# Kernel tuning notes

Measured on AMD Instinct MI355X. Metric: run time of the kernel, lower is better.

The kernel has to match this reference:

```python
import jax, jax.numpy as jnp
import numpy as np

DIM = 128; PDIM = 32; WS = 16; HEADS = 4; NBLK = 2

def gelu(x):
    return jax.nn.gelu(x, approximate=False)  # torch default GELU (erf)

def conv2d(x, w, b=None, pad=0, groups=1):
    y = jax.lax.conv_general_dilated(x, w, (1, 1), [(pad, pad), (pad, pad)],
                                     feature_group_count=groups,
                                     dimension_numbers=('NCHW', 'OIHW', 'NCHW'))
    if b is not None:
        y = y + b[None, :, None, None]
    return y

def layernorm_cf(x, w, b, eps=1e-6):
    # channels_first LayerNorm over C per (b,h,w)
    m = x.mean(axis=1, keepdims=True)
    v = ((x - m) ** 2).mean(axis=1, keepdims=True)
    return (x - m) / jnp.sqrt(v + eps) * w[None, :, None, None] + b[None, :, None, None]

def conv_ffn(x, w1, b1, dw, dwb, w2, b2):
    y = gelu(conv2d(x, w1, b1, 0))
    y = gelu(conv2d(y, dw, dwb, 1, groups=y.shape[1])) + y
    return conv2d(y, w2, b2, 0)

def conv_attention(x, lk, pw1, pb1, pw2, pb2):
    # ConvolutionalAttention (training branch math, non-inplace)
    B, C, H, W = x.shape
    x1, x2 = x[:, :PDIM], x[:, PDIM:]
    # dwc_proj: global avg pool -> 1x1 -> GELU -> 1x1 (pure matmuls on pooled vec)
    v = x1.mean(axis=(2, 3))                              # [B, PDIM]
    h = gelu(v @ pw1[:, :, 0, 0].T + pb1)                 # [B, PDIM//2]
    dk = (h @ pw2[:, :, 0, 0].T + pb2).reshape(B * PDIM, 1, 3, 3)
    # per-sample dynamic depthwise conv via groups = B*PDIM
    dyn = conv2d(x1.reshape(1, B * PDIM, H, W), dk, None, 1,
                 groups=B * PDIM).reshape(B, PDIM, H, W)
    x1 = conv2d(x1, lk, None, lk.shape[-1] // 2) + dyn
    return jnp.concatenate([x1, x2], axis=1)

def window_attention(x, qkv_w, qkv_b, out_w, out_b, table):
    B, C, H, W = x.shape  # H,W divisible by WS -> pad_to_win is a no-op
    hd, wd = H // WS, W // WS
    c = C // HEADS
    qkv = conv2d(x, qkv_w, qkv_b, 0)                      # [B, 3C, H, W]
    qkv = qkv.reshape(B, 3, HEADS, c, hd, WS, wd, WS)
    qkv = qkv.transpose(1, 0, 4, 6, 2, 5, 7, 3).reshape(3, B * hd * wd, HEADS, WS * WS, c)
    q, k, v = qkv[0], qkv[1], qkv[2]
    S = WS * WS
    idx = jnp.arange(S); qh = idx // WS; qw = idx % WS
    rel = (qh[None, :] - qh[:, None] + WS - 1) * (2 * WS - 1) + (qw[None, :] - qw[:, None] + WS - 1)
    bias = table[:, rel]                                  # [HEADS, S, S]
    scores = jnp.einsum('nhqc,nhkc->nhqk', q, k) * (c ** -0.5) + bias[None]
    attn = jax.nn.softmax(scores, axis=-1)
    o = jnp.einsum('nhqk,nhkc->nhqc', attn, v)
    o = o.reshape(B, hd, wd, HEADS, WS, WS, c).transpose(0, 3, 6, 1, 4, 2, 5).reshape(B, C, H, W)
    return conv2d(o, out_w, out_b, 0)

def forward(x, plk_filter, ln_proj_w, ln_proj_b, proj_w1, proj_b1, proj_dw, proj_dwb,
            proj_w2, proj_b2, ln_attn_w, ln_attn_b, qkv_w, qkv_b, attn_out_w, attn_out_b,
            rpe_table, ffn_w1, ffn_b1, ffn_dw, ffn_dwb, ffn_w2, ffn_b2,
            pk_w1, pk_b1, pk_w2, pk_b2, pk_aggr_w, pk_aggr_b,
            ln_out_w, ln_out_b, co_w, co_b):
    skip = x
    x = layernorm_cf(x, ln_proj_w, ln_proj_b)
    x = conv_ffn(x, proj_w1, proj_b1, proj_dw, proj_dwb, proj_w2, proj_b2)
    x = x + window_attention(layernorm_cf(x, ln_attn_w, ln_attn_b),
                             qkv_w, qkv_b, attn_out_w, attn_out_b, rpe_table)
    for i in range(NBLK):
        y = conv_ffn(x, ffn_w1[i], ffn_b1[i], ffn_dw[i], ffn_dwb[i], ffn_w2[i], ffn_b2[i])
        y = conv_attention(y, plk_filter, pk_w1[i], pk_b1[i], pk_w2[i], pk_b2[i])
        y = conv2d(y, pk_aggr_w[i], pk_aggr_b[i], 0)
        x = x + y
    x = conv2d(layernorm_cf(x, ln_out_w, ln_out_b), co_w, co_b, 1)
    return x + skip

def setup_inputs() -> dict:
    key = jax.random.key(0)
    ks = iter(jax.random.split(key, 64))
    def rn(shape, s=0.02):
        return jax.random.normal(next(ks), shape, jnp.float32) * s
    d = DIM; e = 2 * d
    return dict(
        x=jax.random.normal(next(ks), (4, d, 192, 192), jnp.float32),
        plk_filter=rn((PDIM, PDIM, 13, 13), 0.05),
        ln_proj_w=jnp.ones((d,), jnp.float32), ln_proj_b=jnp.zeros((d,), jnp.float32),
        proj_w1=rn((e, d, 1, 1)), proj_b1=rn((e,)),
        proj_dw=rn((e, 1, 3, 3), 0.1), proj_dwb=rn((e,)),
        proj_w2=rn((d, e, 1, 1)), proj_b2=rn((d,)),
        ln_attn_w=jnp.ones((d,), jnp.float32), ln_attn_b=jnp.zeros((d,), jnp.float32),
        qkv_w=rn((3 * d, d, 1, 1)), qkv_b=rn((3 * d,)),
        attn_out_w=rn((d, d, 1, 1)), attn_out_b=rn((d,)),
        rpe_table=rn((HEADS, (2 * WS - 1) ** 2), 0.001),
        ffn_w1=rn((NBLK, e, d, 1, 1)), ffn_b1=rn((NBLK, e)),
        ffn_dw=rn((NBLK, e, 1, 3, 3), 0.1), ffn_dwb=rn((NBLK, e)),
        ffn_w2=rn((NBLK, d, e, 1, 1)), ffn_b2=rn((NBLK, d)),
        pk_w1=rn((NBLK, PDIM // 2, PDIM, 1, 1)), pk_b1=rn((NBLK, PDIM // 2)),
        pk_w2=rn((NBLK, PDIM * 9, PDIM // 2, 1, 1), 0.01), pk_b2=rn((NBLK, PDIM * 9), 0.01),
        pk_aggr_w=rn((NBLK, d, d, 1, 1)), pk_aggr_b=rn((NBLK, d)),
        ln_out_w=jnp.ones((d,), jnp.float32), ln_out_b=jnp.zeros((d,), jnp.float32),
        co_w=rn((d, d, 3, 3), 0.05), co_b=rn((d,)),
    )

def reference(x, plk_filter, ln_proj_w, ln_proj_b, proj_w1, proj_b1, proj_dw, proj_dwb,
              proj_w2, proj_b2, ln_attn_w, ln_attn_b, qkv_w, qkv_b, attn_out_w, attn_out_b,
              rpe_table, ffn_w1, ffn_b1, ffn_dw, ffn_dwb, ffn_w2, ffn_b2,
              pk_w1, pk_b1, pk_w2, pk_b2, pk_aggr_w, pk_aggr_b,
              ln_out_w, ln_out_b, co_w, co_b):
    return forward(x, plk_filter, ln_proj_w, ln_proj_b, proj_w1, proj_b1, proj_dw, proj_dwb,
                   proj_w2, proj_b2, ln_attn_w, ln_attn_b, qkv_w, qkv_b, attn_out_w, attn_out_b,
                   rpe_table, ffn_w1, ffn_b1, ffn_dw, ffn_dwb, ffn_w2, ffn_b2,
                   pk_w1, pk_b1, pk_w2, pk_b2, pk_aggr_w, pk_aggr_b,
                   ln_out_w, ln_out_b, co_w, co_b)
```

## Files before the change

### kernel.cpp

```cpp
#include <hip/hip_runtime.h>
#include <cmath>

#define HWD 192
#define PIX (HWD*HWD)
#define BB  4
#define CCH 128

using short8 = __attribute__((ext_vector_type(8))) short;
using f32x4  = __attribute__((ext_vector_type(4))) float;

__device__ __forceinline__ float gelu_f(float x) {
    return 0.5f * x * (1.0f + erff(x * 0.70710678118654752f));
}
__device__ __forceinline__ unsigned short f2bf(float f) {
    unsigned int u = __float_as_uint(f);
    u += 0x7fff + ((u >> 16) & 1);
    return (unsigned short)(u >> 16);
}
__device__ __forceinline__ float bf2f(unsigned short s) {
    return __uint_as_float((unsigned int)s << 16);
}
__device__ __forceinline__ unsigned short to_bf(float v) { return f2bf(v); }
__device__ __forceinline__ unsigned short to_bf(unsigned short v) { return v; }
__device__ __forceinline__ unsigned pack2bf(float a, float b) {
    return (unsigned)f2bf(a) | ((unsigned)f2bf(b) << 16);
}

__global__ __launch_bounds__(256) void ln_kernel(const float* __restrict__ in,
        const float* __restrict__ w, const float* __restrict__ b,
        unsigned short* __restrict__ out)
{
    int t = blockIdx.x * 256 + threadIdx.x;
    int bi = t / PIX;
    int p  = t - bi*PIX;
    const float* base = in + (size_t)bi * CCH * PIX + p;
    float v[CCH];
    float s = 0.f;
    #pragma unroll
    for (int c=0;c<CCH;++c) { v[c] = base[(size_t)c*PIX]; s += v[c]; }
    float m = s * (1.f/128.f);
    float q = 0.f;
    #pragma unroll
    for (int c=0;c<CCH;++c) { float d = v[c]-m; q += d*d; }
    float iv = rsqrtf(q*(1.f/128.f) + 1e-6f);
    unsigned short* ob = out + (size_t)bi * CCH * PIX + p;
    #pragma unroll
    for (int c=0;c<CCH;++c)
        ob[(size_t)c*PIX] = f2bf((v[c]-m)*iv*w[c] + b[c]);
}

__global__ __launch_bounds__(256) void ln_t_kernel(const float* __restrict__ in,
        const float* __restrict__ w, const float* __restrict__ b,
        unsigned short* __restrict__ outT)
{
    int t = blockIdx.x * 256 + threadIdx.x;
    int bi = t / PIX;
    int p  = t - bi*PIX;
    const float* base = in + (size_t)bi * CCH * PIX + p;
    float v[CCH];
    float s = 0.f;
    #pragma unroll
    for (int c=0;c<CCH;++c) { v[c] = base[(size_t)c*PIX]; s += v[c]; }
    float m = s * (1.f/128.f);
    float q = 0.f;
    #pragma unroll
    for (int c=0;c<CCH;++c) { float d = v[c]-m; q += d*d; }
    float iv = rsqrtf(q*(1.f/128.f) + 1e-6f);
    unsigned short* ob = outT + ((size_t)bi * PIX + p) * 128;
    #pragma unroll
    for (int qq=0; qq<16; ++qq) {
        unsigned short e[8];
        #pragma unroll
        for (int j=0;j<8;++j) {
            int c = qq*8 + j;
            e[j] = f2bf((v[c]-m)*iv*w[c] + b[c]);
        }
        *(uint4*)&ob[qq*8] = *(uint4*)e;
    }
}

__global__ __launch_bounds__(256) void t32_kernel(const unsigned short* __restrict__ in,
    unsigned short* __restrict__ outT)
{
    int t = blockIdx.x * 256 + threadIdx.x;
    int bi = t / PIX;
    int p  = t - bi*PIX;
    const unsigned short* base = in + (size_t)bi * CCH * PIX + p;
    unsigned short e[32];
    #pragma unroll
    for (int c=0;c<32;++c) e[c] = base[(size_t)c*PIX];
    unsigned short* ob = outT + ((size_t)bi * PIX + p) * 32;
    #pragma unroll
    for (int q=0;q<4;++q) *(uint4*)&ob[q*8] = *(uint4*)&e[q*8];
}

template<typename TIN, bool DOGELU, bool DORES, bool OBF>
__global__ __launch_bounds__(256) void conv1x1_mfma_kernel(
    const TIN* __restrict__ in,
    const unsigned short* __restrict__ wq,
    const float* __restrict__ bias,
    const float* __restrict__ res,
    void* __restrict__ outv,
    int Cin)
{
    constexpr int CIP = 72;
    __shared__ unsigned short XL[128*CIP];
    const int Cout = gridDim.y * 128;
    const int px0 = blockIdx.x * 128;
    const int co0 = blockIdx.y * 128;
    const size_t bi = blockIdx.z;
    in  += bi * (size_t)Cin * PIX;
    if (DORES) res += bi * (size_t)Cout * PIX;
    float* outf = (float*)outv + bi * (size_t)Cout * PIX;
    unsigned short* outb = (unsigned short*)outv + bi * (size_t)Cout * PIX;
    const int tid = threadIdx.x;
    const int lane = tid & 63, wid = tid >> 6;
    const int wco = (wid >> 1) * 64;
    const int wpx = (wid & 1) * 64;
    const int l15 = lane & 15, l4 = lane >> 4;

    f32x4 acc[4][4];
    #pragma unroll
    for (int i=0;i<4;++i)
        #pragma unroll
        for (int j=0;j<4;++j) acc[i][j] = (f32x4){0.f,0.f,0.f,0.f};

    for (int k0 = 0; k0 < Cin; k0 += 64) {
        __syncthreads();
        #pragma unroll
        for (int it = 0; it < 8; ++it) {
            int f = tid + it*256;
            int px = f & 127;
            int ci = (f >> 7) * 4;
            const TIN* gp = in + (size_t)(k0+ci)*PIX + px0 + px;
            unsigned short b0 = to_bf(gp[0]);
            unsigned short b1 = to_bf(gp[PIX]);
            unsigned short b2 = to_bf(gp[2*PIX]);
            unsigned short b3 = to_bf(gp[3*PIX]);
            uint2 pk;
            pk.x = (unsigned)b0 | ((unsigned)b1 << 16);
            pk.y = (unsigned)b2 | ((unsigned)b3 << 16);
            *(uint2*)&XL[px*CIP + ci] = pk;
        }
        __syncthreads();
        #pragma unroll
        for (int ks = 0; ks < 2; ++ks) {
            short8 a[4];
            #pragma unroll
            for (int mt=0; mt<4; ++mt) {
                int co = co0 + wco + mt*16 + l15;
                a[mt] = *(const short8*)(wq + (size_t)co*Cin + k0 + ks*32 + l4*8);
            }
            #pragma unroll
            for (int nt=0; nt<4; ++nt) {
                const short8 b = *(const short8*)&XL[(wpx + nt*16 + l15)*CIP + ks*32 + l4*8];
                #pragma unroll
                for (int mt=0; mt<4; ++mt)
                    acc[mt][nt] = __builtin_amdgcn_mfma_f32_16x16x32_bf16(a[mt], b, acc[mt][nt], 0, 0, 0);
            }
        }
    }
    #pragma unroll
    for (int mt=0; mt<4; ++mt) {
        #pragma unroll
        for (int r=0; r<4; ++r) {
            int co = co0 + wco + mt*16 + l4*4 + r;
            float bs = bias[co];
            #pragma unroll
            for (int nt=0; nt<4; ++nt) {
                int px = px0 + wpx + nt*16 + l15;
                float v = acc[mt][nt][r] + bs;
                if (DOGELU) v = gelu_f(v);
                size_t o = (size_t)co*PIX + px;
                if (DORES) v += res[o];
                if (OBF) outb[o] = f2bf(v);
                else     outf[o] = v;
            }
        }
    }
}

__global__ __launch_bounds__(256) void conv3x3_mfma_kernel(
    const unsigned short* __restrict__ inT,
    const unsigned short* __restrict__ wq,
    const float* __restrict__ bias, const float* __restrict__ skip,
    float* __restrict__ out)
{
    constexpr int CIP = 40;
    __shared__ unsigned short XL[4*66*CIP];
    const int x0 = blockIdx.x * 64;
    const int y0 = blockIdx.y * 2;
    const int bi = blockIdx.z;
    const int tid = threadIdx.x;
    const int lane = tid & 63, wid = tid >> 6;
    const int wco = (wid >> 1) * 64;
    const int wrow = wid & 1;
    const int l15 = lane & 15, l4 = lane >> 4;
    const unsigned short* inb = inT + (size_t)bi * PIX * 128;

    f32x4 acc[4][4];
    #pragma unroll
    for (int i=0;i<4;++i)
        #pragma unroll
        for (int j=0;j<4;++j) acc[i][j] = (f32x4){0.f,0.f,0.f,0.f};

    for (int ci0 = 0; ci0 < 128; ci0 += 32) {
        __syncthreads();
        #pragma unroll
        for (int it = 0; it < 5; ++it) {
            int idx = tid + it*256;
            if (idx < 1056) {
                int P = idx >> 2;
                int q = idx & 3;
                int row = P / 66;
                int x = P - row*66;
                int gy = y0 - 1 + row, gx = x0 - 1 + x;
                uint4 v = {0u,0u,0u,0u};
                if ((unsigned)gy < (unsigned)HWD && (unsigned)gx < (unsigned)HWD)
                    v = *(const uint4*)&inb[((size_t)gy*HWD + gx)*128 + ci0 + q*8];
                *(uint4*)&XL[(row*66 + x)*CIP + q*8] = v;
            }
        }
        __syncthreads();
        #pragma unroll
        for (int dy=0; dy<3; ++dy) {
            #pragma unroll
            for (int dx=0; dx<3; ++dx) {
                short8 a[4];
                #pragma unroll
                for (int mt=0; mt<4; ++mt) {
                    int co = wco + mt*16 + l15;
                    a[mt] = *(const short8*)(wq + ((size_t)co*9 + dy*3+dx)*128 + ci0 + l4*8);
                }
                const int rl = wrow + dy;
                #pragma unroll
                for (int nt=0; nt<4; ++nt) {
                    const int xl = nt*16 + l15 + dx;
                    const short8 b = *(const short8*)&XL[(rl*66 + xl)*CIP + l4*8];
                    #pragma unroll
                    for (int mt=0; mt<4; ++mt)
                        acc[mt][nt] = __builtin_amdgcn_mfma_f32_16x16x32_bf16(a[mt], b, acc[mt][nt], 0, 0, 0);
                }
            }
        }
    }
    const int gy = y0 + wrow;
    #pragma unroll
    for (int mt=0; mt<4; ++mt) {
        #pragma unroll
        for (int r=0; r<4; ++r) {
            int co = wco + mt*16 + l4*4 + r;
            float bs = bias[co];
            #pragma unroll
            for (int nt=0; nt<4; ++nt) {
                int gx = x0 + nt*16 + l15;
                size_t o = ((size_t)bi*CCH + co)*PIX + (size_t)gy*HWD + gx;
                out[o] = acc[mt][nt][r] + bs + skip[o];
            }
        }
    }
}

__global__ __launch_bounds__(256) void conv13_mfma_kernel(
    const unsigned short* __restrict__ YT,
    const unsigned short* __restrict__ wq,
    const float* __restrict__ dk,
    unsigned short* __restrict__ outC)
{
    __shared__ unsigned short XL[16*76*32];
    const int x0 = blockIdx.x * 64;
    const int y0 = blockIdx.y * 4;
    const int bi = blockIdx.z;
    const int tid = threadIdx.x;
    const int lane = tid & 63, wr = tid >> 6;
    const int l15 = lane & 15, l4 = lane >> 4;
    const unsigned short* inT = YT + (size_t)bi * PIX * 32;

    #pragma unroll 1
    for (int it = 0; it < 19; ++it) {
        int idx = tid + it*256;
        int P = idx >> 2;
        int q = idx & 3;
        int row = P / 76;
        int x   = P - row*76;
        int gy = y0 - 6 + row, gx = x0 - 6 + x;
        uint4 v = {0u,0u,0u,0u};
        if ((unsigned)gy < (unsigned)HWD && (unsigned)gx < (unsigned)HWD)
            v = *(const uint4*)&inT[((size_t)gy*HWD + gx)*32 + q*8];
        *(uint4*)&XL[P*32 + ((q*8) ^ ((P&3)<<3))] = v;
    }
    __syncthreads();

    f32x4 acc[2][4];
    #pragma unroll
    for (int i=0;i<2;++i)
        #pragma unroll
        for (int j=0;j<4;++j) acc[i][j] = (f32x4){0.f,0.f,0.f,0.f};

    #pragma unroll 1
    for (int dy=0; dy<13; ++dy) {
        const unsigned short* wrow = wq + (size_t)dy*13*1024;
        #pragma unroll
        for (int dx=0; dx<13; ++dx) {
            const short8 a0 = *(const short8*)(wrow + dx*1024 + l15*32 + l4*8);
            const short8 a1 = *(const short8*)(wrow + dx*1024 + (16+l15)*32 + l4*8);
            #pragma unroll
            for (int nt=0; nt<4; ++nt) {
                const int P = (wr + dy)*76 + nt*16 + l15 + dx;
                const short8 b = *(const short8*)&XL[P*32 + ((l4*8) ^ ((P&3)<<3))];
                acc[0][nt] = __builtin_amdgcn_mfma_f32_16x16x32_bf16(a0, b, acc[0][nt], 0, 0, 0);
                acc[1][nt] = __builtin_amdgcn_mfma_f32_16x16x32_bf16(a1, b, acc[1][nt], 0, 0, 0);
            }
        }
    }
    const int gy = y0 + wr;
    #pragma unroll
    for (int mt=0; mt<2; ++mt) {
        #pragma unroll
        for (int r=0; r<4; ++r) {
            const int co = mt*16 + l4*4 + r;
            const float* dkk = dk + (bi*32 + co)*9;
            float k0=dkk[0],k1=dkk[1],k2=dkk[2],k3=dkk[3],k4=dkk[4],
                  k5=dkk[5],k6=dkk[6],k7=dkk[7],k8=dkk[8];
            #pragma unroll
            for (int nt=0; nt<4; ++nt) {
                const int px = nt*16 + l15;
                float dsum = 0.f;
                #pragma unroll
                for (int e=0; e<9; ++e) {
                    int ey = e/3, ex = e - ey*3;
                    int P = (wr+5+ey)*76 + px+5+ex;
                    float pv = bf2f(XL[P*32 + (co ^ ((P&3)<<3))]);
                    float kk = (e==0?k0:e==1?k1:e==2?k2:e==3?k3:e==4?k4:e==5?k5:e==6?k6:e==7?k7:k8);
                    dsum += pv * kk;
                }
                float v = acc[mt][nt][r] + dsum;
                outC[((size_t)bi*32 + co)*PIX + (size_t)gy*HWD + x0 + px] = f2bf(v);
            }
        }
    }
}

__global__ __launch_bounds__(256) void dw3x3_bf_kernel(const unsigned short* __restrict__ in,
    const float* __restrict__ w, const float* __restrict__ b,
    unsigned short* __restrict__ out)
{
    int t = blockIdx.x*256 + threadIdx.x;
    int pc = t / (PIX/4);
    int p4 = (t - pc*(PIX/4)) * 4;
    int c = pc & 255;
    int y = p4 / HWD, x0 = p4 - y*HWD;
    const unsigned short* ib = in + (size_t)pc * PIX;
    float wk[9];
    #pragma unroll
    for (int e=0;e<9;++e) wk[e] = w[c*9+e];
    float bc = b[c];
    float a0=bc,a1=bc,a2=bc,a3=bc;
    #pragma unroll
    for (int ky=0;ky<3;++ky) {
        int yy = y + ky - 1;
        if ((unsigned)yy < (unsigned)HWD) {
            const unsigned short* row = ib + (size_t)yy*HWD;
            float v[6];
            #pragma unroll
            for (int d=0;d<6;++d) {
                int xx = x0 + d - 1;
                v[d] = ((unsigned)xx < (unsigned)HWD) ? bf2f(row[xx]) : 0.f;
            }
            a0 += v[0]*wk[ky*3+0] + v[1]*wk[ky*3+1] + v[2]*wk[ky*3+2];
            a1 += v[1]*wk[ky*3+0] + v[2]*wk[ky*3+1] + v[3]*wk[ky*3+2];
            a2 += v[2]*wk[ky*3+0] + v[3]*wk[ky*3+1] + v[4]*wk[ky*3+2];
            a3 += v[3]*wk[ky*3+0] + v[4]*wk[ky*3+1] + v[5]*wk[ky*3+2];
        }
    }
    const unsigned short* cen = ib + (size_t)y*HWD + x0;
    unsigned short r0 = f2bf(gelu_f(a0) + bf2f(cen[0]));
    unsigned short r1 = f2bf(gelu_f(a1) + bf2f(cen[1]));
    unsigned short r2 = f2bf(gelu_f(a2) + bf2f(cen[2]));
    unsigned short r3 = f2bf(gelu_f(a3) + bf2f(cen[3]));
    uint2 pk;
    pk.x = (unsigned)r0 | ((unsigned)r1 << 16);
    pk.y = (unsigned)r2 | ((unsigned)r3 << 16);
    *(uint2*)(out + (size_t)pc*PIX + p4) = pk;
}

__global__ __launch_bounds__(256) void attn_mfma_kernel(
    const unsigned short* __restrict__ qkv,
    const float* __restrict__ table,
    unsigned short* __restrict__ o)
{
    __shared__ unsigned short KL[256*40];
    __shared__ unsigned short VL[32*264];
    __shared__ unsigned short PL[4*16*264];
    __shared__ float BT[961];
    __shared__ unsigned short OL[64*33];
    const int win = blockIdx.x, head = blockIdx.y;
    const int bi2 = blockIdx.z >> 2, qc = blockIdx.z & 3;
    const int wy = win/12, wx = win - wy*12;
    qkv += (size_t)bi2 * 384 * PIX;
    o   += (size_t)bi2 * CCH * PIX;
    const unsigned short* qb = qkv + (size_t)(head*32) * PIX;
    const unsigned short* kb = qkv + (size_t)(128 + head*32) * PIX;
    const unsigned short* vb = qkv + (size_t)(256 + head*32) * PIX;
    const int tid = threadIdx.x;

    for (int i = tid; i < 8192; i += 256) {
        int c = i >> 8, k = i & 255;
        int sp = ((wy<<4) + (k>>4))*HWD + (wx<<4) + (k&15);
        unsigned short kv = kb[(size_t)c*PIX + sp];
        unsigned short vv = vb[(size_t)c*PIX + sp];
        KL[k*40 + c] = kv;
        VL[c*264 + k] = vv;
    }
    for (int i = tid; i < 961; i += 256) BT[i] = table[head*961 + i];
    __syncthreads();

    const int lane = tid & 63, w = tid >> 6;
    const int l15 = lane & 15, l4 = lane >> 4;
    const int qi = qc*64 + w*16 + l15;
    const int iy = qi >> 4, ix = qi & 15;
    const int spq = ((wy<<4) + iy)*HWD + (wx<<4) + ix;

    short8 qf;
    #pragma unroll
    for (int j=0;j<8;++j) qf[j] = (short)qb[(size_t)(l4*8+j)*PIX + spq];

    f32x4 s[16];
    #pragma unroll
    for (int nt=0; nt<16; ++nt) {
        const short8 a = *(const short8*)&KL[(nt*16 + l15)*40 + l4*8];
        s[nt] = __builtin_amdgcn_mfma_f32_16x16x32_bf16(a, qf, (f32x4){0.f,0.f,0.f,0.f}, 0, 0, 0);
    }

    const float scale = 0.17677669529663687f;
    float m = -1e30f;
    #pragma unroll
    for (int nt=0; nt<16; ++nt) {
        #pragma unroll
        for (int r=0; r<4; ++r) {
            int k = nt*16 + l4*4 + r;
            float bv = BT[((k>>4) - iy + 15)*31 + ((k&15) - ix + 15)];
            float v = s[nt][r]*scale + bv;
            s[nt][r] = v;
            m = fmaxf(m, v);
        }
    }
    m = fmaxf(m, __shfl_xor(m, 16, 64));
    m = fmaxf(m, __shfl_xor(m, 32, 64));
    float l = 0.f;
    #pragma unroll
    for (int nt=0; nt<16; ++nt) {
        #pragma unroll
        for (int r=0; r<4; ++r) {
            float p = __expf(s[nt][r] - m);
            s[nt][r] = p;
            l += p;
        }
    }
    l += __shfl_xor(l, 16, 64);
    l += __shfl_xor(l, 32, 64);

    unsigned short* PLw = &PL[w*16*264];
    #pragma unroll
    for (int nt=0; nt<16; ++nt) {
        *(unsigned*)&PLw[l15*264 + nt*16 + l4*4]     = pack2bf(s[nt][0], s[nt][1]);
        *(unsigned*)&PLw[l15*264 + nt*16 + l4*4 + 2] = pack2bf(s[nt][2], s[nt][3]);
    }

    f32x4 o0 = (f32x4){0.f,0.f,0.f,0.f}, o1 = (f32x4){0.f,0.f,0.f,0.f};
    #pragma unroll
    for (int kt=0; kt<8; ++kt) {
        const short8 pa = *(const short8*)&PLw[l15*264 + kt*32 + l4*8];
        const short8 v0 = *(const short8*)&VL[l15*264 + kt*32 + l4*8];
        const short8 v1 = *(const short8*)&VL[(16+l15)*264 + kt*32 + l4*8];
        o0 = __builtin_amdgcn_mfma_f32_16x16x32_bf16(pa, v0, o0, 0, 0, 0);
        o1 = __builtin_amdgcn_mfma_f32_16x16x32_bf16(pa, v1, o1, 0, 0, 0);
    }

    #pragma unroll
    for (int r=0; r<4; ++r) {
        float lr = __shfl(l, l4*4 + r, 64);
        float inv = 1.f / lr;
        OL[(w*16 + l4*4 + r)*33 + l15]      = f2bf(o0[r]*inv);
        OL[(w*16 + l4*4 + r)*33 + 16 + l15] = f2bf(o1[r]*inv);
    }
    __syncthreads();

    const int d = tid >> 3, seg = tid & 7;
    const int q0l = seg*8;
    const int qi0 = qc*64 + q0l;
    const int sp0 = ((wy<<4) + (qi0>>4))*HWD + (wx<<4) + (qi0 & 15);
    unsigned short tmp[8];
    #pragma unroll
    for (int j=0;j<8;++j) tmp[j] = OL[(q0l+j)*33 + d];
    *(uint4*)&o[(size_t)(head*32 + d)*PIX + sp0] = *(uint4*)tmp;
}

__global__ __launch_bounds__(256) void meanpool_kernel(const unsigned short* __restrict__ in,
    float* __restrict__ v)
{
    int bc = blockIdx.x;
    int bi = bc >> 5, c = bc & 31;
    const unsigned short* base = in + ((size_t)bi*CCH + c) * PIX;
    float s = 0.f;
    for (int i = threadIdx.x; i < PIX/4; i += 256) {
        const uint2 t4 = ((const uint2*)base)[i];
        s += bf2f((unsigned short)(t4.x & 0xffff)) + bf2f((unsigned short)(t4.x >> 16))
           + bf2f((unsigned short)(t4.y & 0xffff)) + bf2f((unsigned short)(t4.y >> 16));
    }
    #pragma unroll
    for (int off=32; off>0; off>>=1) s += __shfl_down(s, off, 64);
    __shared__ float red[4];
    if ((threadIdx.x & 63) == 0) red[threadIdx.x >> 6] = s;
    __syncthreads();
    if (threadIdx.x == 0) v[bc] = (red[0]+red[1]+red[2]+red[3]) * (1.f/PIX);
}

__global__ __launch_bounds__(256) void mlp_kernel(const float* __restrict__ v,
    const float* __restrict__ pw1, const float* __restrict__ pb1,
    const float* __restrict__ pw2, const float* __restrict__ pb2,
    float* __restrict__ dk)
{
    __shared__ float h[64];
    int tid = threadIdx.x;
    if (tid < 64) {
        int bi = tid >> 4, m = tid & 15;
        float s = pb1[m];
        for (int c=0;c<32;++c) s += v[bi*32+c]*pw1[m*32+c];
        h[tid] = gelu_f(s);
    }
    __syncthreads();
    for (int idx = tid; idx < BB*288; idx += 256) {
        int bi = idx / 288, j = idx - bi*288;
        float s = pb2[j];
        for (int m=0;m<16;++m) s += h[bi*16+m]*pw2[j*16+m];
        dk[idx] = s;
    }
}

__global__ __launch_bounds__(256) void wcast_kernel(const float* __restrict__ w,
    unsigned short* __restrict__ wq, int n)
{
    int idx = blockIdx.x*256 + threadIdx.x;
    if (idx < n) wq[idx] = f2bf(w[idx]);
}

__global__ __launch_bounds__(256) void w3cast_kernel(const float* __restrict__ w,
    unsigned short* __restrict__ wq)
{
    int idx = blockIdx.x*256 + threadIdx.x;
    if (idx >= 128*128*9) return;
    int co = idx / (128*9);
    int rem = idx - co*128*9;
    int ci = rem / 9;
    int tap = rem - ci*9;
    wq[((size_t)co*9 + tap)*128 + ci] = f2bf(w[idx]);
}

__global__ __launch_bounds__(256) void w13cast_kernel(const float* __restrict__ w,
    unsigned short* __restrict__ wq)
{
    int idx = blockIdx.x*256 + threadIdx.x;
    if (idx >= 32*32*169) return;
    int co = idx / (32*169);
    int rem = idx - co*32*169;
    int ci = rem / 169;
    int tap = rem - ci*169;
    wq[((size_t)tap*32 + co)*32 + ci] = f2bf(w[idx]);
}

__global__ __launch_bounds__(256) void copyslice_kernel(const unsigned short* __restrict__ src,
    unsigned short* __restrict__ dst)
{
    int idx = blockIdx.x*256 + threadIdx.x;
    int bc = idx / (PIX/8);
    int p8 = (idx - bc*(PIX/8)) * 8;
    int bi = bc >> 5, c = bc & 31;
    *(uint4*)(dst + ((size_t)bi*CCH + c)*PIX + p8) =
        *(const uint4*)(src + (size_t)bc*PIX + p8);
}

extern "C" void kernel_launch(void* const* d_in, const int* in_sizes, int n_in,
                              void* d_out, int out_size, void* d_ws, size_t ws_size,
                              hipStream_t stream) {
    (void)in_sizes; (void)n_in; (void)out_size;
    const float* x_in      = (const float*)d_in[0];
    const float* plk       = (const float*)d_in[1];
    const float* ln_proj_w = (const float*)d_in[2];
    const float* ln_proj_b = (const float*)d_in[3];
    const float* proj_w1   = (const float*)d_in[4];
    const float* proj_b1   = (const float*)d_in[5];
    const float* proj_dw   = (const float*)d_in[6];
    const float* proj_dwb  = (const float*)d_in[7];
    const float* proj_w2   = (const float*)d_in[8];
    const float* proj_b2   = (const float*)d_in[9];
    const float* ln_attn_w = (const float*)d_in[10];
    const float* ln_attn_b = (const float*)d_in[11];
    const float* qkv_w     = (const float*)d_in[12];
    const float* qkv_b     = (const float*)d_in[13];
    const float* attn_ow   = (const float*)d_in[14];
    const float* attn_ob   = (const float*)d_in[15];
    const float* rpe       = (const float*)d_in[16];
    const float* ffn_w1    = (const float*)d_in[17];
    const float* ffn_b1    = (const float*)d_in[18];
    const float* ffn_dw    = (const float*)d_in[19];
    const float* ffn_dwb   = (const float*)d_in[20];
    const float* ffn_w2    = (const float*)d_in[21];
    const float* ffn_b2    = (const float*)d_in[22];
    const float* pk_w1     = (const float*)d_in[23];
    const float* pk_b1     = (const float*)d_in[24];
    const float* pk_w2     = (const float*)d_in[25];
    const float* pk_b2     = (const float*)d_in[26];
    const float* aggr_w    = (const float*)d_in[27];
    const float* aggr_b    = (const float*)d_in[28];
    const float* ln_out_w  = (const float*)d_in[29];
    const float* ln_out_b  = (const float*)d_in[30];
    const float* co_w      = (const float*)d_in[31];
    const float* co_b      = (const float*)d_in[32];
    float* out = (float*)d_out;

    const size_t N1b = (size_t)CCH * PIX;
    const size_t RBsz = (size_t)BB * N1b;
    const size_t LNYw = RBsz / 2;
    const size_t POOLw = RBsz;
    const size_t need_floats = RBsz + LNYw + POOLw + 1408 + 307712 + 64;
    if (ws_size < need_floats * sizeof(float)) return;

    float* ws  = (float*)d_ws;
    float* RB  = ws;
    unsigned short* LNY  = (unsigned short*)(RB + RBsz);
    unsigned short* POOL = (unsigned short*)(RB + RBsz + LNYw);
    float* VB  = (float*)(RB + RBsz + LNYw + POOLw);
    float* DK  = VB + 256;
    unsigned short* Q0  = (unsigned short*)(DK + 1152);
    unsigned short* qPW1 = Q0;
    unsigned short* qPW2 = qPW1 + 32768;
    unsigned short* qQKV = qPW2 + 32768;
    unsigned short* qAT  = qQKV + 49152;
    unsigned short* qF1  = qAT  + 16384;
    unsigned short* qF2  = qF1  + 65536;
    unsigned short* qAG  = qF2  + 65536;
    unsigned short* qW3  = qAG  + 32768;
    unsigned short* qW13 = qW3  + 147456;

    unsigned short* E1 = POOL;
    unsigned short* E2 = POOL + (size_t)2*256*PIX;
    unsigned short* QKV = POOL;
    unsigned short* C13 = POOL;
    unsigned short* YT  = POOL + (size_t)BB*32*PIX;
    unsigned short* XT  = POOL;

    dim3 blk(256);

    wcast_kernel<<<128, blk, 0, stream>>>(proj_w1, qPW1, 32768);
    wcast_kernel<<<128, blk, 0, stream>>>(proj_w2, qPW2, 32768);
    wcast_kernel<<<192, blk, 0, stream>>>(qkv_w, qQKV, 49152);
    wcast_kernel<<<64,  blk, 0, stream>>>(attn_ow, qAT, 16384);
    wcast_kernel<<<256, blk, 0, stream>>>(ffn_w1, qF1, 65536);
    wcast_kernel<<<256, blk, 0, stream>>>(ffn_w2, qF2, 65536);
    wcast_kernel<<<128, blk, 0, stream>>>(aggr_w, qAG, 32768);
    w3cast_kernel<<<576, blk, 0, stream>>>(co_w, qW3);
    w13cast_kernel<<<676, blk, 0, stream>>>(plk, qW13);

    ln_kernel<<<576, blk, 0, stream>>>(x_in, ln_proj_w, ln_proj_b, LNY);
    for (int h=0; h<2; ++h) {
        conv1x1_mfma_kernel<unsigned short,true,false,true><<<dim3(288,2,2), blk, 0, stream>>>(
            LNY + (size_t)h*2*N1b, qPW1, proj_b1, nullptr, E1, 128);
        dw3x3_bf_kernel<<<18432, blk, 0, stream>>>(E1, proj_dw, proj_dwb, E2);
        conv1x1_mfma_kernel<unsigned short,false,false,false><<<dim3(288,1,2), blk, 0, stream>>>(
            E2, qPW2, proj_b2, nullptr, RB + (size_t)h*2*N1b, 256);
    }

    ln_kernel<<<576, blk, 0, stream>>>(RB, ln_attn_w, ln_attn_b, LNY);
    for (int h=0; h<2; ++h) {
        conv1x1_mfma_kernel<unsigned short,false,false,true><<<dim3(288,3,2), blk, 0, stream>>>(
            LNY + (size_t)h*2*N1b, qQKV, qkv_b, nullptr, QKV, 128);
        attn_mfma_kernel<<<dim3(144,4,8), blk, 0, stream>>>(QKV, rpe, LNY + (size_t)h*2*N1b);
    }
    conv1x1_mfma_kernel<unsigned short,false,true,false><<<dim3(288,1,BB), blk, 0, stream>>>(
        LNY, qAT, attn_ob, RB, RB, 128);

    for (int i=0;i<2;++i) {
        const float* fb1 = ffn_b1 + (size_t)i*256;
        const float* fdw = ffn_dw + (size_t)i*256*9;
        const float* fdb = ffn_dwb + (size_t)i*256;
        const float* fb2 = ffn_b2 + (size_t)i*128;
        const float* w1i = pk_w1 + (size_t)i*16*32;
        const float* b1i = pk_b1 + (size_t)i*16;
        const float* w2i = pk_w2 + (size_t)i*288*16;
        const float* b2i = pk_b2 + (size_t)i*288;
        const float* abi = aggr_b + (size_t)i*128;

        for (int h=0; h<2; ++h) {
            conv1x1_mfma_kernel<float,true,false,true><<<dim3(288,2,2), blk, 0, stream>>>(
                RB + (size_t)h*2*N1b, qF1 + (size_t)i*32768, fb1, nullptr, E1, 128);
            dw3x3_bf_kernel<<<18432, blk, 0, stream>>>(E1, fdw, fdb, E2);
            conv1x1_mfma_kernel<unsigned short,false,false,true><<<dim3(288,1,2), blk, 0, stream>>>(
                E2, qF2 + (size_t)i*32768, fb2, nullptr, LNY + (size_t)h*2*N1b, 256);
        }
        t32_kernel<<<576, blk, 0, stream>>>(LNY, YT);
        meanpool_kernel<<<BB*32, blk, 0, stream>>>(LNY, VB);
        mlp_kernel<<<1, blk, 0, stream>>>(VB, w1i, b1i, w2i, b2i, DK);
        conv13_mfma_kernel<<<dim3(3,48,BB), blk, 0, stream>>>(YT, qW13, DK, C13);
        copyslice_kernel<<<(BB*32*(PIX/8))/256, blk, 0, stream>>>(C13, LNY);
        conv1x1_mfma_kernel<unsigned short,false,true,false><<<dim3(288,1,BB), blk, 0, stream>>>(
            LNY, qAG + (size_t)i*16384, abi, RB, RB, 128);
    }

    ln_t_kernel<<<576, blk, 0, stream>>>(RB, ln_out_w, ln_out_b, XT);
    conv3x3_mfma_kernel<<<dim3(3,96,BB), blk, 0, stream>>>(XT, qW3, co_b, x_in, out);
}
```

Before: 1.620 ms.

## Fuse transpose and slice copy into convs, widen K tiles, vectorize loads

```diff
diff --git a/kernel.cpp b/kernel.cpp
--- a/kernel.cpp
+++ b/kernel.cpp
@@ -20,8 +20,6 @@
 __device__ __forceinline__ float bf2f(unsigned short s) {
     return __uint_as_float((unsigned int)s << 16);
 }
-__device__ __forceinline__ unsigned short to_bf(float v) { return f2bf(v); }
-__device__ __forceinline__ unsigned short to_bf(unsigned short v) { return v; }
 __device__ __forceinline__ unsigned pack2bf(float a, float b) {
     return (unsigned)f2bf(a) | ((unsigned)f2bf(b) << 16);
 }
@@ -79,31 +77,17 @@
     }
 }
 
-__global__ __launch_bounds__(256) void t32_kernel(const unsigned short* __restrict__ in,
-    unsigned short* __restrict__ outT)
-{
-    int t = blockIdx.x * 256 + threadIdx.x;
-    int bi = t / PIX;
-    int p  = t - bi*PIX;
-    const unsigned short* base = in + (size_t)bi * CCH * PIX + p;
-    unsigned short e[32];
-    #pragma unroll
-    for (int c=0;c<32;++c) e[c] = base[(size_t)c*PIX];
-    unsigned short* ob = outT + ((size_t)bi * PIX + p) * 32;
-    #pragma unroll
-    for (int q=0;q<4;++q) *(uint4*)&ob[q*8] = *(uint4*)&e[q*8];
-}
-
-template<typename TIN, bool DOGELU, bool DORES, bool OBF>
+template<typename TIN, bool DOGELU, bool DORES, bool OBF, bool WRT32>
 __global__ __launch_bounds__(256) void conv1x1_mfma_kernel(
     const TIN* __restrict__ in,
     const unsigned short* __restrict__ wq,
     const float* __restrict__ bias,
     const float* __restrict__ res,
     void* __restrict__ outv,
+    unsigned short* __restrict__ yt,
     int Cin)
 {
-    constexpr int CIP = 72;
+    constexpr int CIP = 136;
     __shared__ unsigned short XL[128*CIP];
     const int Cout = gridDim.y * 128;
     const int px0 = blockIdx.x * 128;
@@ -111,6 +95,7 @@
     const size_t bi = blockIdx.z;
     in  += bi * (size_t)Cin * PIX;
     if (DORES) res += bi * (size_t)Cout * PIX;
+    if (WRT32) yt += bi * (size_t)PIX * 32;
     float* outf = (float*)outv + bi * (size_t)Cout * PIX;
     unsigned short* outb = (unsigned short*)outv + bi * (size_t)Cout * PIX;
     const int tid = threadIdx.x;
@@ -125,26 +110,38 @@
         #pragma unroll
         for (int j=0;j<4;++j) acc[i][j] = (f32x4){0.f,0.f,0.f,0.f};
 
-    for (int k0 = 0; k0 < Cin; k0 += 64) {
+    for (int k0 = 0; k0 < Cin; k0 += 128) {
         __syncthreads();
         #pragma unroll
-        for (int it = 0; it < 8; ++it) {
-            int f = tid + it*256;
-            int px = f & 127;
-            int ci = (f >> 7) * 4;
-            const TIN* gp = in + (size_t)(k0+ci)*PIX + px0 + px;
-            unsigned short b0 = to_bf(gp[0]);
-            unsigned short b1 = to_bf(gp[PIX]);
-            unsigned short b2 = to_bf(gp[2*PIX]);
-            unsigned short b3 = to_bf(gp[3*PIX]);
-            uint2 pk;
-            pk.x = (unsigned)b0 | ((unsigned)b1 << 16);
-            pk.y = (unsigned)b2 | ((unsigned)b3 << 16);
-            *(uint2*)&XL[px*CIP + ci] = pk;
+        for (int it = 0; it < 4; ++it) {
+            int idx = tid + it*256;
+            int c2  = idx & 63;
+            int s   = idx >> 6;
+            const TIN* g0 = in + (size_t)(k0 + c2*2    )*PIX + px0 + s*8;
+            const TIN* g1 = in + (size_t)(k0 + c2*2 + 1)*PIX + px0 + s*8;
+            unsigned short a8[8], b8[8];
+            if constexpr (sizeof(TIN) == 2) {
+                *(uint4*)a8 = *(const uint4*)g0;
+                *(uint4*)b8 = *(const uint4*)g1;
+            } else {
+                const float4 f0 = *(const float4*)g0;
+                const float4 f1 = *(const float4*)(g0+4);
+                const float4 f2 = *(const float4*)g1;
+                const float4 f3 = *(const float4*)(g1+4);
+                a8[0]=f2bf(f0.x); a8[1]=f2bf(f0.y); a8[2]=f2bf(f0.z); a8[3]=f2bf(f0.w);
+                a8[4]=f2bf(f1.x); a8[5]=f2bf(f1.y); a8[6]=f2bf(f1.z); a8[7]=f2bf(f1.w);
+                b8[0]=f2bf(f2.x); b8[1]=f2bf(f2.y); b8[2]=f2bf(f2.z); b8[3]=f2bf(f2.w);
+                b8[4]=f2bf(f3.x); b8[5]=f2bf(f3.y); b8[6]=f2bf(f3.z); b8[7]=f2bf(f3.w);
+            }
+            #pragma unroll
+            for (int j=0;j<8;++j) {
+                unsigned pk = (unsigned)a8[j] | ((unsigned)b8[j] << 16);
+                *(unsigned*)&XL[(s*8+j)*CIP + c2*2] = pk;
+            }
         }
         __syncthreads();
         #pragma unroll
-        for (int ks = 0; ks < 2; ++ks) {
+        for (int ks = 0; ks < 4; ++ks) {
             short8 a[4];
             #pragma unroll
             for (int mt=0; mt<4; ++mt) {
@@ -173,8 +170,11 @@
                 if (DOGELU) v = gelu_f(v);
                 size_t o = (size_t)co*PIX + px;
                 if (DORES) v += res[o];
-                if (OBF) outb[o] = f2bf(v);
-                else     outf[o] = v;
+                if (OBF) {
+                    unsigned short bv = f2bf(v);
+                    outb[o] = bv;
+                    if (WRT32 && co < 32) yt[(size_t)px*32 + co] = bv;
+                } else outf[o] = v;
             }
         }
     }
@@ -186,7 +186,7 @@
     const float* __restrict__ bias, const float* __restrict__ skip,
     float* __restrict__ out)
 {
-    constexpr int CIP = 40;
+    constexpr int CIP = 72;
     __shared__ unsigned short XL[4*66*CIP];
     const int x0 = blockIdx.x * 64;
     const int y0 = blockIdx.y * 2;
@@ -204,21 +204,21 @@
         #pragma unroll
         for (int j=0;j<4;++j) acc[i][j] = (f32x4){0.f,0.f,0.f,0.f};
 
-    for (int ci0 = 0; ci0 < 128; ci0 += 32) {
+    for (int ci0 = 0; ci0 < 128; ci0 += 64) {
         __syncthreads();
         #pragma unroll
-        for (int it = 0; it < 5; ++it) {
+        for (int it = 0; it < 9; ++it) {
             int idx = tid + it*256;
-            if (idx < 1056) {
-                int P = idx >> 2;
-                int q = idx & 3;
+            if (idx < 2112) {
+                int P = idx >> 3;
+                int q = idx & 7;
                 int row = P / 66;
                 int x = P - row*66;
                 int gy = y0 - 1 + row, gx = x0 - 1 + x;
                 uint4 v = {0u,0u,0u,0u};
                 if ((unsigned)gy < (unsigned)HWD && (unsigned)gx < (unsigned)HWD)
                     v = *(const uint4*)&inb[((size_t)gy*HWD + gx)*128 + ci0 + q*8];
-                *(uint4*)&XL[(row*66 + x)*CIP + q*8] = v;
+                *(uint4*)&XL[P*CIP + q*8] = v;
             }
         }
         __syncthreads();
@@ -226,20 +226,23 @@
         for (int dy=0; dy<3; ++dy) {
             #pragma unroll
             for (int dx=0; dx<3; ++dx) {
-                short8 a[4];
-                #pragma unroll
-                for (int mt=0; mt<4; ++mt) {
-                    int co = wco + mt*16 + l15;
-                    a[mt] = *(const short8*)(wq + ((size_t)co*9 + dy*3+dx)*128 + ci0 + l4*8);
-                }
                 const int rl = wrow + dy;
                 #pragma unroll
-                for (int nt=0; nt<4; ++nt) {
-                    const int xl = nt*16 + l15 + dx;
-                    const short8 b = *(const short8*)&XL[(rl*66 + xl)*CIP + l4*8];
+                for (int ks=0; ks<2; ++ks) {
+                    short8 a[4];
                     #pragma unroll
-                    for (int mt=0; mt<4; ++mt)
-                        acc[mt][nt] = __builtin_amdgcn_mfma_f32_16x16x32_bf16(a[mt], b, acc[mt][nt], 0, 0, 0);
+                    for (int mt=0; mt<4; ++mt) {
+                        int co = wco + mt*16 + l15;
+                        a[mt] = *(const short8*)(wq + ((size_t)co*9 + dy*3+dx)*128 + ci0 + ks*32 + l4*8);
+                    }
+                    #pragma unroll
+                    for (int nt=0; nt<4; ++nt) {
+                        const int xl = nt*16 + l15 + dx;
+                        const short8 b = *(const short8*)&XL[(rl*66 + xl)*CIP + ks*32 + l4*8];
+                        #pragma unroll
+                        for (int mt=0; mt<4; ++mt)
+                            acc[mt][nt] = __builtin_amdgcn_mfma_f32_16x16x32_bf16(a[mt], b, acc[mt][nt], 0, 0, 0);
+                    }
                 }
             }
         }
@@ -265,7 +268,7 @@
     const unsigned short* __restrict__ YT,
     const unsigned short* __restrict__ wq,
     const float* __restrict__ dk,
-    unsigned short* __restrict__ outC)
+    unsigned short* __restrict__ outL)
 {
     __shared__ unsigned short XL[16*76*32];
     const int x0 = blockIdx.x * 64;
@@ -335,7 +338,7 @@
                     dsum += pv * kk;
                 }
                 float v = acc[mt][nt][r] + dsum;
-                outC[((size_t)bi*32 + co)*PIX + (size_t)gy*HWD + x0 + px] = f2bf(v);
+                outL[((size_t)bi*CCH + co)*PIX + (size_t)gy*HWD + x0 + px] = f2bf(v);
             }
         }
     }
@@ -404,13 +407,18 @@
     const unsigned short* vb = qkv + (size_t)(256 + head*32) * PIX;
     const int tid = threadIdx.x;
 
+    #pragma unroll
+    for (int it = 0; it < 4; ++it) {
+        int idx = tid + it*256;
+        int c = idx >> 5, seg = idx & 31;
+        int k0 = seg*8;
+        int sp = ((wy<<4) + (k0>>4))*HWD + (wx<<4) + (k0&15);
+        *(uint4*)&VL[c*264 + k0] = *(const uint4*)&vb[(size_t)c*PIX + sp];
+    }
     for (int i = tid; i < 8192; i += 256) {
         int c = i >> 8, k = i & 255;
         int sp = ((wy<<4) + (k>>4))*HWD + (wx<<4) + (k&15);
-        unsigned short kv = kb[(size_t)c*PIX + sp];
-        unsigned short vv = vb[(size_t)c*PIX + sp];
-        KL[k*40 + c] = kv;
-        VL[c*264 + k] = vv;
+        KL[k*40 + c] = kb[(size_t)c*PIX + sp];
     }
     for (int i = tid; i < 961; i += 256) BT[i] = table[head*961 + i];
     __syncthreads();
@@ -567,17 +575,6 @@
     int ci = rem / 169;
     int tap = rem - ci*169;
     wq[((size_t)tap*32 + co)*32 + ci] = f2bf(w[idx]);
-}
-
-__global__ __launch_bounds__(256) void copyslice_kernel(const unsigned short* __restrict__ src,
-    unsigned short* __restrict__ dst)
-{
-    int idx = blockIdx.x*256 + threadIdx.x;
-    int bc = idx / (PIX/8);
-    int p8 = (idx - bc*(PIX/8)) * 8;
-    int bi = bc >> 5, c = bc & 31;
-    *(uint4*)(dst + ((size_t)bi*CCH + c)*PIX + p8) =
-        *(const uint4*)(src + (size_t)bc*PIX + p8);
 }
 
 extern "C" void kernel_launch(void* const* d_in, const int* in_sizes, int n_in,
@@ -623,14 +620,16 @@
     const size_t RBsz = (size_t)BB * N1b;
     const size_t LNYw = RBsz / 2;
     const size_t POOLw = RBsz;
-    const size_t need_floats = RBsz + LNYw + POOLw + 1408 + 307712 + 64;
+    const size_t YTw  = (size_t)BB*PIX*32/2;
+    const size_t need_floats = RBsz + LNYw + POOLw + YTw + 256 + 1152 + 307712 + 64;
     if (ws_size < need_floats * sizeof(float)) return;
 
     float* ws  = (float*)d_ws;
     float* RB  = ws;
     unsigned short* LNY  = (unsigned short*)(RB + RBsz);
     unsigned short* POOL = (unsigned short*)(RB + RBsz + LNYw);
-    float* VB  = (float*)(RB + RBsz + LNYw + POOLw);
+    unsigned short* YT   = (unsigned short*)(RB + RBsz + LNYw + POOLw);
+    float* VB  = (float*)(RB + RBsz + LNYw + POOLw + YTw);
     float* DK  = VB + 256;
     unsigned short* Q0  = (unsigned short*)(DK + 1152);
     unsigned short* qPW1 = Q0;
@@ -646,8 +645,6 @@
     unsigned short* E1 = POOL;
     unsigned short* E2 = POOL + (size_t)2*256*PIX;
     unsigned short* QKV = POOL;
-    unsigned short* C13 = POOL;
-    unsigned short* YT  = POOL + (size_t)BB*32*PIX;
     unsigned short* XT  = POOL;
 
     dim3 blk(256);
@@ -664,21 +661,21 @@
 
     ln_kernel<<<576, blk, 0, stream>>>(x_in, ln_proj_w, ln_proj_b, LNY);
     for (int h=0; h<2; ++h) {
-        conv1x1_mfma_kernel<unsigned short,true,false,true><<<dim3(288,2,2), blk, 0, stream>>>(
-            LNY + (size_t)h*2*N1b, qPW1, proj_b1, nullptr, E1, 128);
+        conv1x1_mfma_kernel<unsigned short,true,false,true,false><<<dim3(288,2,2), blk, 0, stream>>>(
+            LNY + (size_t)h*2*N1b, qPW1, proj_b1, nullptr, E1, nullptr, 128);
         dw3x3_bf_kernel<<<18432, blk, 0, stream>>>(E1, proj_dw, proj_dwb, E2);
-        conv1x1_mfma_kernel<unsigned short,false,false,false><<<dim3(288,1,2), blk, 0, stream>>>(
-            E2, qPW2, proj_b2, nullptr, RB + (size_t)h*2*N1b, 256);
+        conv1x1_mfma_kernel<unsigned short,false,false,false,false><<<dim3(288,1,2), blk, 0, stream>>>(
+            E2, qPW2, proj_b2, nullptr, RB + (size_t)h*2*N1b, nullptr, 256);
     }
 
     ln_kernel<<<576, blk, 0, stream>>>(RB, ln_attn_w, ln_attn_b, LNY);
     for (int h=0; h<2; ++h) {
-        conv1x1_mfma_kernel<unsigned short,false,false,true><<<dim3(288,3,2), blk, 0, stream>>>(
-            LNY + (size_t)h*2*N1b, qQKV, qkv_b, nullptr, QKV, 128);
+        conv1x1_mfma_kernel<unsigned short,false,false,true,false><<<dim3(288,3,2), blk, 0, stream>>>(
+            LNY + (size_t)h*2*N1b, qQKV, qkv_b, nullptr, QKV, nullptr, 128);
         attn_mfma_kernel<<<dim3(144,4,8), blk, 0, stream>>>(QKV, rpe, LNY + (size_t)h*2*N1b);
     }
-    conv1x1_mfma_kernel<unsigned short,false,true,false><<<dim3(288,1,BB), blk, 0, stream>>>(
-        LNY, qAT, attn_ob, RB, RB, 128);
+    conv1x1_mfma_kernel<unsigned short,false,true,false,false><<<dim3(288,1,BB), blk, 0, stream>>>(
+        LNY, qAT, attn_ob, RB, RB, nullptr, 128);
 
     for (int i=0;i<2;++i) {
         const float* fb1 = ffn_b1 + (size_t)i*256;
@@ -692,19 +689,18 @@
         const float* abi = aggr_b + (size_t)i*128;
 
         for (int h=0; h<2; ++h) {
-            conv1x1_mfma_kernel<float,true,false,true><<<dim3(288,2,2), blk, 0, stream>>>(
-                RB + (size_t)h*2*N1b, qF1 + (size_t)i*32768, fb1, nullptr, E1, 128);
+            conv1x1_mfma_kernel<float,true,false,true,false><<<dim3(288,2,2), blk, 0, stream>>>(
+                RB + (size_t)h*2*N1b, qF1 + (size_t)i*32768, fb1, nullptr, E1, nullptr, 128);
             dw3x3_bf_kernel<<<18432, blk, 0, stream>>>(E1, fdw, fdb, E2);
-            conv1x1_mfma_kernel<unsigned short,false,false,true><<<dim3(288,1,2), blk, 0, stream>>>(
-                E2, qF2 + (size_t)i*32768, fb2, nullptr, LNY + (size_t)h*2*N1b, 256);
-        }
-        t32_kernel<<<576, blk, 0, stream>>>(LNY, YT);
+            conv1x1_mfma_kernel<unsigned short,false,false,true,true><<<dim3(288,1,2), blk, 0, stream>>>(
+                E2, qF2 + (size_t)i*32768, fb2, nullptr, LNY + (size_t)h*2*N1b,
+                YT + (size_t)h*2*PIX*32, 256);
+        }
         meanpool_kernel<<<BB*32, blk, 0, stream>>>(LNY, VB);
         mlp_kernel<<<1, blk, 0, stream>>>(VB, w1i, b1i, w2i, b2i, DK);
-        conv13_mfma_kernel<<<dim3(3,48,BB), blk, 0, stream>>>(YT, qW13, DK, C13);
-        copyslice_kernel<<<(BB*32*(PIX/8))/256, blk, 0, stream>>>(C13, LNY);
-        conv1x1_mfma_kernel<unsigned short,false,true,false><<<dim3(288,1,BB), blk, 0, stream>>>(
-            LNY, qAG + (size_t)i*16384, abi, RB, RB, 128);
+        conv13_mfma_kernel<<<dim3(3,48,BB), blk, 0, stream>>>(YT, qW13, DK, LNY);
+        conv1x1_mfma_kernel<unsigned short,false,true,false,false><<<dim3(288,1,BB), blk, 0, stream>>>(
+            LNY, qAG + (size_t)i*16384, abi, RB, RB, nullptr, 128);
     }
 
     ln_t_kernel<<<576, blk, 0, stream>>>(RB, ln_out_w, ln_out_b, XT);
```

New measurement: 1.651 ms. Within noise of the previous version (+2.0%).
